# Kernel optimization log

Hardware: AMD Instinct MI355X
Metric: run time of the kernel (lower is better)

Reference implementation:

```python
import jax, jax.numpy as jnp
import numpy as np

N_NODES = 100000
IN_CH = 65
HID_CH = 64
N_EDGES = 3200000


def setup_inputs() -> dict:
    key = jax.random.key(0)
    k1, k2, k3, k4, k5 = jax.random.split(key, 5)
    x = jax.random.normal(k1, (N_NODES, IN_CH), dtype=jnp.float32)
    edge_index = jax.random.randint(k2, (2, N_EDGES), 0, N_NODES, dtype=jnp.int64)
    edge_weight = jax.random.uniform(k3, (N_EDGES,), dtype=jnp.float32)
    # PyG GraphConv params: lin_rel (with bias) applied to aggregated neighbors,
    # lin_root (no bias) applied to self features.
    scale = 1.0 / np.sqrt(IN_CH)
    W_rel = jax.random.uniform(k4, (HID_CH, IN_CH), dtype=jnp.float32, minval=-scale, maxval=scale)
    b_rel = jnp.zeros((HID_CH,), dtype=jnp.float32)
    W_root = jax.random.uniform(k5, (HID_CH, IN_CH), dtype=jnp.float32, minval=-scale, maxval=scale)
    return {"x": x, "edge_index": edge_index, "edge_weight": edge_weight,
            "W_rel": W_rel, "b_rel": b_rel, "W_root": W_root}


def reference(x, edge_index, edge_weight, W_rel, b_rel, W_root):
    src = edge_index[0]  # source nodes (x_j in PyG message)
    dst = edge_index[1]  # target nodes (aggregation index)
    # gather neighbor features, weight by edge weight: [E, IN_CH]
    msgs = x[src] * edge_weight[:, None]
    # scatter-add to destination nodes: [N, IN_CH]
    aggr = jax.ops.segment_sum(msgs, dst, num_segments=N_NODES)
    # out = lin_rel(aggr) + lin_root(x)
    out = aggr @ W_rel.T + b_rel + x @ W_root.T
    return out
```

## Files before the change

### kernel.cpp

```cpp
#include <hip/hip_runtime.h>

#define IN_CH 65
#define HID 64
#define BN 64
#define NB 1563
#define CAP 2560
#define SCAP 2432
#define GT 2
#define PTPB 512
#define SEPB 8192
#define SEPT (SEPB / PTPB)
#define WSTR 132

static inline size_t align16(size_t v) { return (v + 15) & ~(size_t)15; }

__device__ inline ushort f2bf(float f) {
    uint u = __float_as_uint(f);
    return (ushort)((u + 0x7FFF + ((u >> 16) & 1)) >> 16);
}

__global__ __launch_bounds__(PTPB) void prep(const float* __restrict__ x,
                                             const float* __restrict__ W_rel,
                                             const float* __restrict__ W_root,
                                             const float* __restrict__ b_rel,
                                             ushort* __restrict__ y16,
                                             float* __restrict__ out,
                                             const int* __restrict__ ei,
                                             const float* __restrict__ ew,
                                             int* __restrict__ cnt,
                                             int2* __restrict__ pairs,
                                             int nNodes, int nTiles, int E) {
    __shared__ __align__(16) char smem[3 * 65 * 68 * 4];
    const int bid = blockIdx.x;
    const int s3 = bid / 3, r3 = bid - s3 * 3;
    const int tid = threadIdx.x;

    if (r3 != 2) {
        const int gblk = s3 * 2 + r3;
        const int sub = tid >> 8;
        const int t256 = tid & 255;
        const int tile = gblk * GT + sub;
        float* xsT = (float*)smem + sub * (65 * 68);
        float* ws  = (float*)smem + 2 * (65 * 68);
        const int tx = t256 & 15;
        const int ty = t256 >> 4;
        const long nodeBase = (long)tile * 64;
        const int nValid = (int)min((long)64, (long)nNodes - nodeBase);

        for (int f = tid; f < HID * IN_CH; f += PTPB) {
            const int j = f / IN_CH, c = f - j * IN_CH;
            ws[c * 68 + j] = W_rel[f];
        }
        const float* xsrc = x + nodeBase * IN_CH;
        for (int f = t256; f < 64 * IN_CH; f += 256) {
            const int node = f / IN_CH, k = f - node * IN_CH;
            xsT[k * 68 + node] = (node < nValid) ? xsrc[f] : 0.f;
        }
        __syncthreads();

        const int r0 = ty * 4;
        const int c0 = tx * 4;

        {
            float acc[4][4];
#pragma unroll
            for (int i = 0; i < 4; ++i)
#pragma unroll
                for (int j = 0; j < 4; ++j) acc[i][j] = 0.f;

            for (int k = 0; k < IN_CH; ++k) {
                const float4 a4 = *(const float4*)&xsT[k * 68 + r0];
                const float4 b4 = *(const float4*)&ws[k * 68 + c0];
                const float aa[4] = {a4.x, a4.y, a4.z, a4.w};
                const float bb[4] = {b4.x, b4.y, b4.z, b4.w};
#pragma unroll
                for (int i = 0; i < 4; ++i)
#pragma unroll
                    for (int j = 0; j < 4; ++j) acc[i][j] += aa[i] * bb[j];
            }
#pragma unroll
            for (int i = 0; i < 4; ++i) {
                const long node = nodeBase + r0 + i;
                if (node >= nNodes) break;
                uint2 pk;
                pk.x = (uint)f2bf(acc[i][0]) | ((uint)f2bf(acc[i][1]) << 16);
                pk.y = (uint)f2bf(acc[i][2]) | ((uint)f2bf(acc[i][3]) << 16);
                *(uint2*)&y16[node * HID + c0] = pk;
            }
        }
        __syncthreads();

        for (int f = tid; f < HID * IN_CH; f += PTPB) {
            const int j = f / IN_CH, c = f - j * IN_CH;
            ws[c * 68 + j] = W_root[f];
        }
        __syncthreads();

        {
            const float4 bb4 = *(const float4*)&b_rel[c0];
            float acc[4][4];
#pragma unroll
            for (int i = 0; i < 4; ++i) {
                acc[i][0] = bb4.x; acc[i][1] = bb4.y;
                acc[i][2] = bb4.z; acc[i][3] = bb4.w;
            }
            for (int k = 0; k < IN_CH; ++k) {
                const float4 a4 = *(const float4*)&xsT[k * 68 + r0];
                const float4 b4 = *(const float4*)&ws[k * 68 + c0];
                const float aa[4] = {a4.x, a4.y, a4.z, a4.w};
                const float bb[4] = {b4.x, b4.y, b4.z, b4.w};
#pragma unroll
                for (int i = 0; i < 4; ++i)
#pragma unroll
                    for (int j = 0; j < 4; ++j) acc[i][j] += aa[i] * bb[j];
            }
#pragma unroll
            for (int i = 0; i < 4; ++i) {
                const long node = nodeBase + r0 + i;
                if (node >= nNodes) break;
                *(float4*)&out[node * HID + c0] =
                    make_float4(acc[i][0], acc[i][1], acc[i][2], acc[i][3]);
            }
        }
    } else {
        int* lhist = (int*)smem;
        int* lbase = lhist + NB;
        const long e0 = (long)s3 * SEPB;
        const int n = (int)min((long)SEPB, (long)E - e0);

        for (int i = tid; i < NB; i += PTPB) lhist[i] = 0;
        __syncthreads();

        int dstv[SEPT], srcv[SEPT];
        float wv[SEPT];
#pragma unroll
        for (int k = 0; k < SEPT; ++k) {
            const int i = tid + k * PTPB;
            const bool valid = i < n;
            dstv[k] = valid ? ei[(long)E + e0 + i] : 0;
            srcv[k] = valid ? ei[e0 + i] : 0;
            wv[k]   = valid ? ew[e0 + i] : 0.f;
            if (valid) atomicAdd(&lhist[dstv[k] >> 6], 1);
        }
        __syncthreads();

        for (int i = tid; i < NB; i += PTPB) {
            const int c = lhist[i];
            lbase[i] = c ? atomicAdd(&cnt[i], c) : 0;
            lhist[i] = 0;
        }
        __syncthreads();

#pragma unroll
        for (int k = 0; k < SEPT; ++k) {
            const int i = tid + k * PTPB;
            if (i < n) {
                const int b = dstv[k] >> 6;
                const int p = lbase[b] + atomicAdd(&lhist[b], 1);
                if (p < CAP)
                    pairs[(size_t)b * CAP + p] =
                        make_int2((srcv[k] << 7) | ((dstv[k] & (BN - 1)) << 25),
                                  __float_as_int(wv[k]));
            }
        }
    }
}

__global__ __launch_bounds__(512) void aggregateS16(const int2* __restrict__ pairs,
                                                    const int* __restrict__ cnt,
                                                    const ushort* __restrict__ y16,
                                                    float* __restrict__ out, int N) {
    __shared__ int2 sorted[SCAP];
    __shared__ int sH[BN];
    __shared__ int soff[BN + 1];
    __shared__ int scur[BN];
    const int tid = threadIdx.x;
    const int lane = tid & 63;
    const int wvid = tid >> 6;
    const int half = lane >> 5;
    const uint lane4 = (lane & 31) * 4;
    const int b = blockIdx.x;

    if (tid < BN) { sH[tid] = 0; scur[tid] = 0; }

    const int m = min(cnt[b], CAP);
    const int2* pb = pairs + (size_t)b * CAP;

    int2 pv[5];
#pragma unroll
    for (int kk = 0; kk < 5; ++kk) {
        const int i = tid + kk * 512;
        if (i < m) pv[kk] = pb[i];
    }
    __syncthreads();

#pragma unroll
    for (int kk = 0; kk < 5; ++kk) {
        const int i = tid + kk * 512;
        if (i < m) atomicAdd(&sH[(uint)pv[kk].x >> 25], 1);
    }
    __syncthreads();

    for (int off = 1; off < BN; off <<= 1) {
        int v = 0;
        if (tid < BN) {
            v = sH[tid];
            if (tid >= off) v += sH[tid - off];
        }
        __syncthreads();
        if (tid < BN) sH[tid] = v;
        __syncthreads();
    }
    if (tid < BN) soff[tid + 1] = sH[tid];
    if (tid == 0) soff[0] = 0;
    __syncthreads();

#pragma unroll
    for (int kk = 0; kk < 5; ++kk) {
        const int i = tid + kk * 512;
        if (i < m) {
            const int d = (uint)pv[kk].x >> 25;
            const int slot = soff[d] + atomicAdd(&scur[d], 1);
            if (slot < SCAP) sorted[slot] = make_int2(pv[kk].x & 0x00FFFF80, pv[kk].y);
        }
    }
    __syncthreads();

    const char* yb = (const char*)y16;
    const long nodeBase = (long)b * BN;
    for (int nl = wvid; nl < BN; nl += 8) {
        const long node = nodeBase + nl;
        if (node >= N) break;
        const int kbeg = min(soff[nl], SCAP);
        const int kend = min(soff[nl + 1], SCAP);
        float2* o = (float2*)(out + node * HID) + (lane & 31);
        const float2 cur = *o;
        float ax = 0.f, ay = 0.f;
        int k = kbeg + half;
        for (; k + 14 < kend; k += 16) {
            int2 pp[8];
#pragma unroll
            for (int j = 0; j < 8; ++j) pp[j] = sorted[k + 2 * j];
            uint qq[8];
#pragma unroll
            for (int j = 0; j < 8; ++j)
                qq[j] = *(const uint*)(yb + (uint)pp[j].x + lane4);
#pragma unroll
            for (int j = 0; j < 8; ++j) {
                const float w = __int_as_float(pp[j].y);
                ax += w * __uint_as_float(qq[j] << 16);
                ay += w * __uint_as_float(qq[j] & 0xFFFF0000u);
            }
        }
        for (; k + 6 < kend; k += 8) {
            const int2 p0 = sorted[k],     p1 = sorted[k + 2];
            const int2 p2 = sorted[k + 4], p3 = sorted[k + 6];
            const uint q0 = *(const uint*)(yb + (uint)p0.x + lane4);
            const uint q1 = *(const uint*)(yb + (uint)p1.x + lane4);
            const uint q2 = *(const uint*)(yb + (uint)p2.x + lane4);
            const uint q3 = *(const uint*)(yb + (uint)p3.x + lane4);
            const float w0 = __int_as_float(p0.y), w1 = __int_as_float(p1.y);
            const float w2 = __int_as_float(p2.y), w3 = __int_as_float(p3.y);
            ax += w0 * __uint_as_float(q0 << 16);
            ay += w0 * __uint_as_float(q0 & 0xFFFF0000u);
            ax += w1 * __uint_as_float(q1 << 16);
            ay += w1 * __uint_as_float(q1 & 0xFFFF0000u);
            ax += w2 * __uint_as_float(q2 << 16);
            ay += w2 * __uint_as_float(q2 & 0xFFFF0000u);
            ax += w3 * __uint_as_float(q3 << 16);
            ay += w3 * __uint_as_float(q3 & 0xFFFF0000u);
        }
        for (; k < kend; k += 2) {
            const int2 p = sorted[k];
            const uint q = *(const uint*)(yb + (uint)p.x + lane4);
            const float w = __int_as_float(p.y);
            ax += w * __uint_as_float(q << 16);
            ay += w * __uint_as_float(q & 0xFFFF0000u);
        }
        ax += __shfl_xor(ax, 32);
        ay += __shfl_xor(ay, 32);
        if (half == 0) {
            *o = make_float2(cur.x + ax, cur.y + ay);
        }
    }
}

__global__ __launch_bounds__(256) void k1_full(const float* __restrict__ x,
                                               const float* __restrict__ W_rel,
                                               const float* __restrict__ b_rel,
                                               const float* __restrict__ W_root,
                                               ushort* __restrict__ y16,
                                               float* __restrict__ out,
                                               int nNodes) {
    __shared__ float xs[64 * IN_CH];
    __shared__ float ws[IN_CH * WSTR];
    const int tid = threadIdx.x;
    const int tx = tid & 15;
    const int ty = tid >> 4;
    const long nodeBase = (long)blockIdx.x * 64;
    const int nValid = min(64, nNodes - (int)nodeBase);
    const int nx = nValid * IN_CH;

    for (int f = tid; f < HID * IN_CH; f += 256) {
        const int j = f / IN_CH, c = f - j * IN_CH;
        ws[c * WSTR + j] = W_rel[f];
    }
    for (int f = tid; f < HID * IN_CH; f += 256) {
        const int j = f / IN_CH, c = f - j * IN_CH;
        ws[c * WSTR + HID + j] = W_root[f];
    }
    const float* xsrc = x + nodeBase * IN_CH;
    for (int i = tid; i < 64 * IN_CH; i += 256) xs[i] = (i < nx) ? xsrc[i] : 0.f;
    __syncthreads();

    float acc[4][8];
#pragma unroll
    for (int i = 0; i < 4; ++i)
#pragma unroll
        for (int j = 0; j < 8; ++j) acc[i][j] = 0.f;

    const int r0 = ty * 4;
    const int c0 = tx * 8;
    for (int k = 0; k < IN_CH; ++k) {
        float aa[4] = {xs[(r0 + 0) * IN_CH + k], xs[(r0 + 1) * IN_CH + k],
                       xs[(r0 + 2) * IN_CH + k], xs[(r0 + 3) * IN_CH + k]};
        float4 b0 = *(const float4*)&ws[k * WSTR + c0];
        float4 b1 = *(const float4*)&ws[k * WSTR + c0 + 4];
        float bb[8] = {b0.x, b0.y, b0.z, b0.w, b1.x, b1.y, b1.z, b1.w};
#pragma unroll
        for (int i = 0; i < 4; ++i)
#pragma unroll
            for (int j = 0; j < 8; ++j) acc[i][j] += aa[i] * bb[j];
    }

    if (c0 >= HID) {
        const int h0 = c0 - HID;
        float4 bb0 = *(const float4*)&b_rel[h0];
        float4 bb1 = *(const float4*)&b_rel[h0 + 4];
        float bv[8] = {bb0.x, bb0.y, bb0.z, bb0.w, bb1.x, bb1.y, bb1.z, bb1.w};
#pragma unroll
        for (int i = 0; i < 4; ++i)
#pragma unroll
            for (int j = 0; j < 8; ++j) acc[i][j] += bv[j];
    }

#pragma unroll
    for (int i = 0; i < 4; ++i) {
        const long node = nodeBase + r0 + i;
        if (node >= nNodes) break;
        if (c0 < HID) {
            uint4 pk;
            pk.x = (uint)f2bf(acc[i][0]) | ((uint)f2bf(acc[i][1]) << 16);
            pk.y = (uint)f2bf(acc[i][2]) | ((uint)f2bf(acc[i][3]) << 16);
            pk.z = (uint)f2bf(acc[i][4]) | ((uint)f2bf(acc[i][5]) << 16);
            pk.w = (uint)f2bf(acc[i][6]) | ((uint)f2bf(acc[i][7]) << 16);
            *(uint4*)&y16[node * HID + c0] = pk;
        } else {
            float* dst = out + node * HID + (c0 - HID);
            *(float4*)(dst + 0) = make_float4(acc[i][0], acc[i][1], acc[i][2], acc[i][3]);
            *(float4*)(dst + 4) = make_float4(acc[i][4], acc[i][5], acc[i][6], acc[i][7]);
        }
    }
}

__global__ __launch_bounds__(256) void k2_atomic16(const int* __restrict__ ei,
                                                   const float* __restrict__ ew,
                                                   const ushort* __restrict__ y16,
                                                   float* __restrict__ out, int E) {
    const long t = (long)blockIdx.x * 256 + threadIdx.x;
    const long e = t >> 4;
    const int r = (int)(t & 15);
    if (e >= E) return;
    const int src = ei[e];
    const int dst = ei[(long)E + e];
    const float w = ew[e];
    const uint2 q = ((const uint2*)y16)[(size_t)src * 16 + r];
    float* o = out + (size_t)dst * HID + r * 4;
    unsafeAtomicAdd(o + 0, w * __uint_as_float(q.x << 16));
    unsafeAtomicAdd(o + 1, w * __uint_as_float(q.x & 0xFFFF0000u));
    unsafeAtomicAdd(o + 2, w * __uint_as_float(q.y << 16));
    unsafeAtomicAdd(o + 3, w * __uint_as_float(q.y & 0xFFFF0000u));
}

extern "C" void kernel_launch(void* const* d_in, const int* in_sizes, int n_in,
                              void* d_out, int out_size, void* d_ws, size_t ws_size,
                              hipStream_t stream) {
    const float* x      = (const float*)d_in[0];
    const int*   ei     = (const int*)d_in[1];
    const float* ew     = (const float*)d_in[2];
    const float* W_rel  = (const float*)d_in[3];
    const float* b_rel  = (const float*)d_in[4];
    const float* W_root = (const float*)d_in[5];
    float* out = (float*)d_out;

    const int N = in_sizes[0] / IN_CH;
    const int E = in_sizes[2];

    char* base = (char*)d_ws;
    const size_t oY     = 0;
    const size_t oPairs = align16((size_t)N * HID * 2);
    const size_t oCnt   = oPairs + align16((size_t)NB * CAP * 8);
    const size_t need   = oCnt + (size_t)NB * 4;

    ushort* y16 = (ushort*)(base + oY);
    const int nTiles = (N + 63) / 64;

    const bool fits = (ws_size >= need) && (N <= (1 << 17)) &&
                      ((size_t)NB * BN >= (size_t)N) && ((long)E <= (long)N * 33);

    if (fits) {
        int2* pairs = (int2*)(base + oPairs);
        int*  cnt   = (int*)(base + oCnt);

        hipMemsetAsync(cnt, 0, (size_t)NB * sizeof(int), stream);

        const int gemmBlocks = (nTiles + GT - 1) / GT;
        const int scatBlocks = (E + SEPB - 1) / SEPB;
        const int nTrip = max((gemmBlocks + 1) / 2, scatBlocks);
        const int grid = nTrip * 3;

        prep<<<grid, PTPB, 0, stream>>>(x, W_rel, W_root, b_rel, y16, out,
                                        ei, ew, cnt, pairs, N, nTiles, E);
        aggregateS16<<<NB, 512, 0, stream>>>(pairs, cnt, y16, out, N);
    } else {
        const int nbf = (N + 63) / 64;
        k1_full<<<nbf, 256, 0, stream>>>(x, W_rel, b_rel, W_root, y16, out, N);
        const long thr2 = (long)E * 16;
        k2_atomic16<<<(int)((thr2 + 255) / 256), 256, 0, stream>>>(ei, ew, y16, out, E);
    }
}
```

Baseline: 226.3 us.

## Fuse memset, prep and aggregate into one cooperative persistent kernel

```diff
diff --git a/kernel.cpp b/kernel.cpp
--- a/kernel.cpp
+++ b/kernel.cpp
@@ -1,4 +1,7 @@
 #include <hip/hip_runtime.h>
+#include <hip/hip_cooperative_groups.h>
+
+namespace cg = cooperative_groups;
 
 #define IN_CH 65
 #define HID 64
@@ -17,6 +20,289 @@
 __device__ inline ushort f2bf(float f) {
     uint u = __float_as_uint(f);
     return (ushort)((u + 0x7FFF + ((u >> 16) & 1)) >> 16);
+}
+
+__global__ __launch_bounds__(PTPB) void fused(const float* __restrict__ x,
+                                              const float* __restrict__ W_rel,
+                                              const float* __restrict__ W_root,
+                                              const float* __restrict__ b_rel,
+                                              ushort* __restrict__ y16,
+                                              float* __restrict__ out,
+                                              const int* __restrict__ ei,
+                                              const float* __restrict__ ew,
+                                              int* __restrict__ cnt,
+                                              int2* __restrict__ pairs,
+                                              int nNodes, int nTiles, int E,
+                                              int NU) {
+    __shared__ __align__(16) char smem[3 * 65 * 68 * 4];
+    cg::grid_group grid = cg::this_grid();
+    const int tid = threadIdx.x;
+    const int sUnits = (E + SEPB - 1) / SEPB;
+    const int gUnits = (nTiles + GT - 1) / GT;
+
+    for (int i = blockIdx.x * PTPB + tid; i < NB; i += gridDim.x * PTPB)
+        cnt[i] = 0;
+    grid.sync();
+
+    for (int u = blockIdx.x; u < NU; u += gridDim.x) {
+        const int trip = u / 3, r = u - trip * 3;
+        if (r == 2) {
+            if (trip < sUnits) {
+                int* lhist = (int*)smem;
+                int* lbase = lhist + NB;
+                const long e0 = (long)trip * SEPB;
+                const int n = (int)min((long)SEPB, (long)E - e0);
+
+                for (int i = tid; i < NB; i += PTPB) lhist[i] = 0;
+                __syncthreads();
+
+                int dstv[SEPT], srcv[SEPT];
+                float wv[SEPT];
+#pragma unroll
+                for (int k = 0; k < SEPT; ++k) {
+                    const int i = tid + k * PTPB;
+                    const bool valid = i < n;
+                    dstv[k] = valid ? ei[(long)E + e0 + i] : 0;
+                    srcv[k] = valid ? ei[e0 + i] : 0;
+                    wv[k]   = valid ? ew[e0 + i] : 0.f;
+                    if (valid) atomicAdd(&lhist[dstv[k] >> 6], 1);
+                }
+                __syncthreads();
+
+                for (int i = tid; i < NB; i += PTPB) {
+                    const int c = lhist[i];
+                    lbase[i] = c ? atomicAdd(&cnt[i], c) : 0;
+                    lhist[i] = 0;
+                }
+                __syncthreads();
+
+#pragma unroll
+                for (int k = 0; k < SEPT; ++k) {
+                    const int i = tid + k * PTPB;
+                    if (i < n) {
+                        const int b = dstv[k] >> 6;
+                        const int p = lbase[b] + atomicAdd(&lhist[b], 1);
+                        if (p < CAP)
+                            pairs[(size_t)b * CAP + p] =
+                                make_int2((srcv[k] << 7) |
+                                          ((dstv[k] & (BN - 1)) << 25),
+                                          __float_as_int(wv[k]));
+                    }
+                }
+            }
+        } else {
+            const int gblk = trip * 2 + r;
+            if (gblk < gUnits) {
+                const int sub = tid >> 8;
+                const int t256 = tid & 255;
+                const int tile = gblk * GT + sub;
+                float* xsT = (float*)smem + sub * (65 * 68);
+                float* ws  = (float*)smem + 2 * (65 * 68);
+                const int tx = t256 & 15;
+                const int ty = t256 >> 4;
+                const long nodeBase = (long)tile * 64;
+                const int nValid = (int)min((long)64, (long)nNodes - nodeBase);
+
+                for (int f = tid; f < HID * IN_CH; f += PTPB) {
+                    const int j = f / IN_CH, c = f - j * IN_CH;
+                    ws[c * 68 + j] = W_rel[f];
+                }
+                const float* xsrc = x + nodeBase * IN_CH;
+                for (int f = t256; f < 64 * IN_CH; f += 256) {
+                    const int node = f / IN_CH, k = f - node * IN_CH;
+                    xsT[k * 68 + node] = (node < nValid) ? xsrc[f] : 0.f;
+                }
+                __syncthreads();
+
+                const int r0 = ty * 4;
+                const int c0 = tx * 4;
+
+                {
+                    float acc[4][4];
+#pragma unroll
+                    for (int i = 0; i < 4; ++i)
+#pragma unroll
+                        for (int j = 0; j < 4; ++j) acc[i][j] = 0.f;
+
+                    for (int k = 0; k < IN_CH; ++k) {
+                        const float4 a4 = *(const float4*)&xsT[k * 68 + r0];
+                        const float4 b4 = *(const float4*)&ws[k * 68 + c0];
+                        const float aa[4] = {a4.x, a4.y, a4.z, a4.w};
+                        const float bb[4] = {b4.x, b4.y, b4.z, b4.w};
+#pragma unroll
+                        for (int i = 0; i < 4; ++i)
+#pragma unroll
+                            for (int j = 0; j < 4; ++j)
+                                acc[i][j] += aa[i] * bb[j];
+                    }
+#pragma unroll
+                    for (int i = 0; i < 4; ++i) {
+                        const long node = nodeBase + r0 + i;
+                        if (node >= nNodes) break;
+                        uint2 pk;
+                        pk.x = (uint)f2bf(acc[i][0]) | ((uint)f2bf(acc[i][1]) << 16);
+                        pk.y = (uint)f2bf(acc[i][2]) | ((uint)f2bf(acc[i][3]) << 16);
+                        *(uint2*)&y16[node * HID + c0] = pk;
+                    }
+                }
+                __syncthreads();
+
+                for (int f = tid; f < HID * IN_CH; f += PTPB) {
+                    const int j = f / IN_CH, c = f - j * IN_CH;
+                    ws[c * 68 + j] = W_root[f];
+                }
+                __syncthreads();
+
+                {
+                    const float4 bb4 = *(const float4*)&b_rel[c0];
+                    float acc[4][4];
+#pragma unroll
+                    for (int i = 0; i < 4; ++i) {
+                        acc[i][0] = bb4.x; acc[i][1] = bb4.y;
+                        acc[i][2] = bb4.z; acc[i][3] = bb4.w;
+                    }
+                    for (int k = 0; k < IN_CH; ++k) {
+                        const float4 a4 = *(const float4*)&xsT[k * 68 + r0];
+                        const float4 b4 = *(const float4*)&ws[k * 68 + c0];
+                        const float aa[4] = {a4.x, a4.y, a4.z, a4.w};
+                        const float bb[4] = {b4.x, b4.y, b4.z, b4.w};
+#pragma unroll
+                        for (int i = 0; i < 4; ++i)
+#pragma unroll
+                            for (int j = 0; j < 4; ++j)
+                                acc[i][j] += aa[i] * bb[j];
+                    }
+#pragma unroll
+                    for (int i = 0; i < 4; ++i) {
+                        const long node = nodeBase + r0 + i;
+                        if (node >= nNodes) break;
+                        *(float4*)&out[node * HID + c0] =
+                            make_float4(acc[i][0], acc[i][1], acc[i][2], acc[i][3]);
+                    }
+                }
+            }
+        }
+        __syncthreads();
+    }
+
+    __threadfence();
+    grid.sync();
+
+    int2* sorted = (int2*)smem;
+    int*  sH     = (int*)(smem + 19456);
+    int*  soff   = sH + BN;
+    int*  scur   = soff + BN + 1;
+    const int lane = tid & 63;
+    const int wvid = tid >> 6;
+    const int half = lane >> 5;
+    const uint lane4 = (lane & 31) * 4;
+    const char* yb = (const char*)y16;
+
+    for (int b = blockIdx.x; b < NB; b += gridDim.x) {
+        if (tid < BN) { sH[tid] = 0; scur[tid] = 0; }
+
+        const int m = min(cnt[b], CAP);
+        const int2* pb = pairs + (size_t)b * CAP;
+
+        int2 pv[5];
+#pragma unroll
+        for (int kk = 0; kk < 5; ++kk) {
+            const int i = tid + kk * 512;
+            if (i < m) pv[kk] = pb[i];
+        }
+        __syncthreads();
+
+#pragma unroll
+        for (int kk = 0; kk < 5; ++kk) {
+            const int i = tid + kk * 512;
+            if (i < m) atomicAdd(&sH[(uint)pv[kk].x >> 25], 1);
+        }
+        __syncthreads();
+
+        for (int off = 1; off < BN; off <<= 1) {
+            int v = 0;
+            if (tid < BN) {
+                v = sH[tid];
+                if (tid >= off) v += sH[tid - off];
+            }
+            __syncthreads();
+            if (tid < BN) sH[tid] = v;
+            __syncthreads();
+        }
+        if (tid < BN) soff[tid + 1] = sH[tid];
+        if (tid == 0) soff[0] = 0;
+        __syncthreads();
+
+#pragma unroll
+        for (int kk = 0; kk < 5; ++kk) {
+            const int i = tid + kk * 512;
+            if (i < m) {
+                const int d = (uint)pv[kk].x >> 25;
+                const int slot = soff[d] + atomicAdd(&scur[d], 1);
+                if (slot < SCAP)
+                    sorted[slot] = make_int2(pv[kk].x & 0x00FFFF80, pv[kk].y);
+            }
+        }
+        __syncthreads();
+
+        const long nodeBase = (long)b * BN;
+        for (int nl = wvid; nl < BN; nl += 8) {
+            const long node = nodeBase + nl;
+            if (node >= nNodes) break;
+            const int kbeg = min(soff[nl], SCAP);
+            const int kend = min(soff[nl + 1], SCAP);
+            float2* o = (float2*)(out + node * HID) + (lane & 31);
+            const float2 cur = *o;
+            float ax = 0.f, ay = 0.f;
+            int k = kbeg + half;
+            for (; k + 14 < kend; k += 16) {
+                int2 pp[8];
+#pragma unroll
+                for (int j = 0; j < 8; ++j) pp[j] = sorted[k + 2 * j];
+                uint qq[8];
+#pragma unroll
+                for (int j = 0; j < 8; ++j)
+                    qq[j] = *(const uint*)(yb + (uint)pp[j].x + lane4);
+#pragma unroll
+                for (int j = 0; j < 8; ++j) {
+                    const float w = __int_as_float(pp[j].y);
+                    ax += w * __uint_as_float(qq[j] << 16);
+                    ay += w * __uint_as_float(qq[j] & 0xFFFF0000u);
+                }
+            }
+            for (; k + 6 < kend; k += 8) {
+                const int2 p0 = sorted[k],     p1 = sorted[k + 2];
+                const int2 p2 = sorted[k + 4], p3 = sorted[k + 6];
+                const uint q0 = *(const uint*)(yb + (uint)p0.x + lane4);
+                const uint q1 = *(const uint*)(yb + (uint)p1.x + lane4);
+                const uint q2 = *(const uint*)(yb + (uint)p2.x + lane4);
+                const uint q3 = *(const uint*)(yb + (uint)p3.x + lane4);
+                const float w0 = __int_as_float(p0.y), w1 = __int_as_float(p1.y);
+                const float w2 = __int_as_float(p2.y), w3 = __int_as_float(p3.y);
+                ax += w0 * __uint_as_float(q0 << 16);
+                ay += w0 * __uint_as_float(q0 & 0xFFFF0000u);
+                ax += w1 * __uint_as_float(q1 << 16);
+                ay += w1 * __uint_as_float(q1 & 0xFFFF0000u);
+                ax += w2 * __uint_as_float(q2 << 16);
+                ay += w2 * __uint_as_float(q2 & 0xFFFF0000u);
+                ax += w3 * __uint_as_float(q3 << 16);
+                ay += w3 * __uint_as_float(q3 & 0xFFFF0000u);
+            }
+            for (; k < kend; k += 2) {
+                const int2 p = sorted[k];
+                const uint q = *(const uint*)(yb + (uint)p.x + lane4);
+                const float w = __int_as_float(p.y);
+                ax += w * __uint_as_float(q << 16);
+                ay += w * __uint_as_float(q & 0xFFFF0000u);
+            }
+            ax += __shfl_xor(ax, 32);
+            ay += __shfl_xor(ay, 32);
+            if (half == 0) {
+                *o = make_float2(cur.x + ax, cur.y + ay);
+            }
+        }
+        __syncthreads();
+    }
 }
 
 __global__ __launch_bounds__(PTPB) void prep(const float* __restrict__ x,
@@ -60,14 +346,12 @@
 
         const int r0 = ty * 4;
         const int c0 = tx * 4;
-
         {
             float acc[4][4];
 #pragma unroll
             for (int i = 0; i < 4; ++i)
 #pragma unroll
                 for (int j = 0; j < 4; ++j) acc[i][j] = 0.f;
-
             for (int k = 0; k < IN_CH; ++k) {
                 const float4 a4 = *(const float4*)&xsT[k * 68 + r0];
                 const float4 b4 = *(const float4*)&ws[k * 68 + c0];
@@ -89,13 +373,11 @@
             }
         }
         __syncthreads();
-
         for (int f = tid; f < HID * IN_CH; f += PTPB) {
             const int j = f / IN_CH, c = f - j * IN_CH;
             ws[c * 68 + j] = W_root[f];
         }
         __syncthreads();
-
         {
             const float4 bb4 = *(const float4*)&b_rel[c0];
             float acc[4][4];
@@ -412,16 +694,47 @@
         int2* pairs = (int2*)(base + oPairs);
         int*  cnt   = (int*)(base + oCnt);
 
-        hipMemsetAsync(cnt, 0, (size_t)NB * sizeof(int), stream);
-
-        const int gemmBlocks = (nTiles + GT - 1) / GT;
-        const int scatBlocks = (E + SEPB - 1) / SEPB;
-        const int nTrip = max((gemmBlocks + 1) / 2, scatBlocks);
-        const int grid = nTrip * 3;
-
-        prep<<<grid, PTPB, 0, stream>>>(x, W_rel, W_root, b_rel, y16, out,
-                                        ei, ew, cnt, pairs, N, nTiles, E);
-        aggregateS16<<<NB, 512, 0, stream>>>(pairs, cnt, y16, out, N);
+        const int sUnits = (E + SEPB - 1) / SEPB;
+        const int gUnits = (nTiles + GT - 1) / GT;
+        const int nTrip = max((gUnits + 1) / 2, sUnits);
+        const int NU = nTrip * 3;
+
+        static int coopGrid = -2;
+        if (coopGrid == -2) {
+            coopGrid = -1;
+            hipDeviceProp_t prop;
+            int occ = 0;
+            if (hipGetDeviceProperties(&prop, 0) == hipSuccess &&
+                prop.cooperativeLaunch &&
+                hipOccupancyMaxActiveBlocksPerMultiprocessor(
+                    &occ, fused, PTPB, 0) == hipSuccess && occ >= 1) {
+                coopGrid = occ * prop.multiProcessorCount;
+                if (coopGrid > 768) coopGrid = 768;
+            }
+        }
+
+        bool launched = false;
+        if (coopGrid >= 256) {
+            const float* xv = x; const float* wrv = W_rel;
+            const float* wov = W_root; const float* brv = b_rel;
+            ushort* yv = y16; float* ov = out;
+            const int* eiv = ei; const float* ewv = ew;
+            int* cntv = cnt; int2* pv = pairs;
+            int Nv = N, nTv = nTiles, Ev = E, NUv = NU;
+            void* kargs[] = {&xv, &wrv, &wov, &brv, &yv, &ov,
+                             &eiv, &ewv, &cntv, &pv, &Nv, &nTv, &Ev, &NUv};
+            launched = (hipLaunchCooperativeKernel((const void*)fused,
+                                                   dim3(coopGrid), dim3(PTPB),
+                                                   kargs, 0, stream) == hipSuccess);
+        }
+
+        if (!launched) {
+            hipMemsetAsync(cnt, 0, (size_t)NB * sizeof(int), stream);
+            const int grid = nTrip * 3;
+            prep<<<grid, PTPB, 0, stream>>>(x, W_rel, W_root, b_rel, y16, out,
+                                            ei, ew, cnt, pairs, N, nTiles, E);
+            aggregateS16<<<NB, 512, 0, stream>>>(pairs, cnt, y16, out, N);
+        }
     } else {
         const int nbf = (N + 63) / 64;
         k1_full<<<nbf, 256, 0, stream>>>(x, W_rel, b_rel, W_root, y16, out, N);
```

After: 225.7 us. Within noise of the previous version (-0.3%).
